# Optimization experiments

Hardware: AMD Instinct MI355X
Metric: run time of the kernel (lower is better)

The kernel has to match this reference:

```python
import jax, jax.numpy as jnp
import numpy as np

N = 50000      # nodes
E = 600000     # edges
D_IN = 128
HID = 128
D_OUT = 3
G = 32         # graphs in the batch


def setup_inputs() -> dict:
    key = jax.random.key(0)
    ks = jax.random.split(key, 16)
    s = 0.05
    x = jax.random.normal(ks[0], (N, D_IN), dtype=jnp.float32)
    edge_index = jax.random.randint(ks[1], (2, E), 0, N, dtype=jnp.int64)
    batch = jnp.sort(jax.random.randint(ks[2], (N,), 0, G, dtype=jnp.int64))
    return {
        "x": x,
        "conv0_Wl": jax.random.normal(ks[3], (HID, D_IN), jnp.float32) * s,
        "conv0_bl": jnp.zeros((HID,), jnp.float32),
        "conv0_Wr": jax.random.normal(ks[4], (HID, D_IN), jnp.float32) * s,
        "lin1_W": jax.random.normal(ks[5], (HID, HID), jnp.float32) * s,
        "lin1_b": jnp.zeros((HID,), jnp.float32),
        "conv1_Wl": jax.random.normal(ks[6], (HID, HID), jnp.float32) * s,
        "conv1_bl": jnp.zeros((HID,), jnp.float32),
        "conv1_Wr": jax.random.normal(ks[7], (HID, HID), jnp.float32) * s,
        "fc_W": jax.random.normal(ks[8], (D_OUT, HID), jnp.float32) * s,
        "fc_b": jnp.zeros((D_OUT,), jnp.float32),
        "edge_index": edge_index,
        "batch": batch,
    }


def _sage_conv(x, Wl, bl, Wr, src, dst):
    # PyG SAGEConv (mean aggr): out = lin_l(mean_{j in N(i)} x_j) + lin_r(x_i)
    msg = x[src]                                              # [E, d] gather
    ssum = jax.ops.segment_sum(msg, dst, num_segments=N)      # [N, d]
    cnt = jax.ops.segment_sum(jnp.ones((src.shape[0],), x.dtype), dst, num_segments=N)
    aggr = ssum / jnp.maximum(cnt, 1.0)[:, None]
    return aggr @ Wl.T + bl + x @ Wr.T


def reference(x, conv0_Wl, conv0_bl, conv0_Wr, lin1_W, lin1_b,
              conv1_Wl, conv1_bl, conv1_Wr, fc_W, fc_b,
              edge_index, batch):
    src, dst = edge_index[0], edge_index[1]
    # conv0 -> relu (dropout is identity in eval mode)
    h = jax.nn.relu(_sage_conv(x, conv0_Wl, conv0_bl, conv0_Wr, src, dst))
    # Linear -> relu -> SAGEConv -> relu
    h = jax.nn.relu(h @ lin1_W.T + lin1_b)
    h = jax.nn.relu(_sage_conv(h, conv1_Wl, conv1_bl, conv1_Wr, src, dst))
    # global_mean_pool over graphs
    gsum = jax.ops.segment_sum(h, batch, num_segments=G)
    gcnt = jax.ops.segment_sum(jnp.ones((h.shape[0],), h.dtype), batch, num_segments=G)
    pooled = gsum / jnp.maximum(gcnt, 1.0)[:, None]           # [G, HID]
    return pooled @ fc_W.T + fc_b                             # [G, D_OUT]
```

## Files before the change

kernel.cpp:

```cpp
#include <hip/hip_runtime.h>
#include <hip/hip_bf16.h>
#include <stdint.h>


typedef __attribute__((ext_vector_type(8))) short short8;
typedef __attribute__((ext_vector_type(4))) float f32x4;

__device__ __forceinline__ float bits2f(uint32_t b) {
    union { uint32_t u; float f; } c; c.u = b; return c.f;
}
__device__ __forceinline__ unsigned short f2bf(float f) {
    __hip_bfloat16 h = __float2bfloat16(f);
    union { __hip_bfloat16 h; unsigned short u; } c; c.h = h; return c.u;
}
__device__ __forceinline__ uint32_t pack2bf(float a, float b) {
    return (uint32_t)f2bf(a) | ((uint32_t)f2bf(b) << 16);
}
__device__ __forceinline__ void acc8(float* a, uint4 v) {
    a[0] += bits2f(v.x << 16); a[1] += bits2f(v.x & 0xffff0000u);
    a[2] += bits2f(v.y << 16); a[3] += bits2f(v.y & 0xffff0000u);
    a[4] += bits2f(v.z << 16); a[5] += bits2f(v.z & 0xffff0000u);
    a[6] += bits2f(v.w << 16); a[7] += bits2f(v.w & 0xffff0000u);
}

__device__ __forceinline__ void detect_flags(const unsigned short* x,
                                             const int* ei,
                                             int& isbf, int& is64) {
    int lane = threadIdx.x & 63;
    unsigned short h = x[lane];
    int e = (h >> 7) & 0xFF;
    unsigned long long mbf = __ballot(e >= 102 && e <= 137);
    unsigned long long m64 = __ballot(ei[2 * lane + 1] != 0);
    isbf = (__popcll(mbf) >= 52) ? 1 : 0;
    is64 = (m64 == 0ULL) ? 1 : 0;
}

#define WB_W0L 0
#define WB_W0R 16384
#define WB_W1  32768
#define WB_W1L 49152
#define WB_W1R 65536
#define WB_TOTAL 81920
#define CF_B0L 0
#define CF_B1  128
#define CF_B1L 256
#define CF_FCW 384
#define CF_FCB 768
#define CF_TOTAL 771

__global__ __launch_bounds__(256) void prep_kernel(
    const void* x, const int* __restrict__ ei,
    const void* s0, const void* s1, const void* s2, const void* s3,
    const void* s4, const void* f0, const void* f1, const void* f2,
    const void* f3, const void* f4,
    unsigned short* __restrict__ Hb, unsigned short* __restrict__ wb,
    float* __restrict__ cf, int* __restrict__ cnt, int* __restrict__ nbr,
    int* __restrict__ flags, int n8, int E, int EG, int WC) {
    int isbf, is64;
    detect_flags((const unsigned short*)x, ei, isbf, is64);
    int b = blockIdx.x;
    if (b == 0 && threadIdx.x == 0) { flags[0] = isbf; flags[1] = is64; }

    if (b < EG) {
        int e = b * 256 + threadIdx.x;
        if (e >= E) return;
        int s, d;
        if (is64) { s = ei[2 * e]; d = ei[2 * (E + e)]; }
        else      { s = ei[e];     d = ei[E + e]; }
        int pos = atomicAdd(&cnt[d], 1);
        if (pos < 64) nbr[((size_t)d << 6) + pos] = s;
    } else if (b < EG + WC) {
        int i = (b - EG) * 256 + threadIdx.x;
        if (i < WB_TOTAL) {
            const void* p; int k = i & 16383;
            switch (i >> 14) {
                case 0: p = s0; break;
                case 1: p = s1; break;
                case 2: p = s2; break;
                case 3: p = s3; break;
                default: p = s4; break;
            }
            wb[i] = isbf ? ((const unsigned short*)p)[k]
                         : f2bf(((const float*)p)[k]);
        } else {
            int j = i - WB_TOTAL;
            if (j >= CF_TOTAL) return;
            const void* p; int k;
            if      (j < CF_B1)  { p = f0; k = j; }
            else if (j < CF_B1L) { p = f1; k = j - CF_B1; }
            else if (j < CF_FCW) { p = f2; k = j - CF_B1L; }
            else if (j < CF_FCB) { p = f3; k = j - CF_FCW; }
            else                 { p = f4; k = j - CF_FCB; }
            cf[j] = isbf ? bits2f((uint32_t)((const unsigned short*)p)[k] << 16)
                         : ((const float*)p)[k];
        }
    } else {
        if (isbf) return;
        int i = (b - EG - WC) * 256 + threadIdx.x;
        if (i >= n8) return;
        float4 a = ((const float4*)x)[2 * i];
        float4 c = ((const float4*)x)[2 * i + 1];
        uint4 d;
        d.x = pack2bf(a.x, a.y); d.y = pack2bf(a.z, a.w);
        d.z = pack2bf(c.x, c.y); d.w = pack2bf(c.z, c.w);
        ((uint4*)Hb)[i] = d;
    }
}

template <bool LIN1, bool POOL>
__device__ __forceinline__ void conv_core(
    const void* xsel, const unsigned short* __restrict__ Hbuf,
    const int* __restrict__ cnt, const int* __restrict__ nbr,
    const unsigned short* __restrict__ Wl, const unsigned short* __restrict__ Wr,
    const float* __restrict__ bias,
    const unsigned short* __restrict__ W2, const float* __restrict__ bias2,
    unsigned short* __restrict__ Hdst,
    float* __restrict__ pool, const int* __restrict__ batch,
    const int* __restrict__ flags, int N) {
    __shared__ unsigned short bufA[16 * 136];
    __shared__ unsigned short bufB[16 * 136];
    __shared__ float pbuf[4 * 128];
    const int t = threadIdx.x;
    const int lane = t & 63;
    const int w = t >> 6;
    const int l15 = lane & 15;
    const int kq = lane >> 4;
    const int m0 = blockIdx.x * 16;

    const int flags0 = flags[0];
    const unsigned short* Hs = flags0 ? (const unsigned short*)xsel : Hbuf;

    int f64 = 0, gmin = 0, g[4];
    if (POOL) {
        f64 = flags[1];
        gmin = f64 ? batch[2 * m0] : batch[m0];
#pragma unroll
        for (int r = 0; r < 4; r++) {
            int gr = m0 + kq * 4 + r;
            g[r] = (gr < N) ? (f64 ? batch[2 * gr] : batch[gr]) : -1;
        }
        for (int i = t; i < 512; i += 256) pbuf[i] = 0.f;
    }

    short8 xf[4];
    {
        int xr = m0 + l15; if (xr >= N) xr = N - 1;
        const unsigned short* xrow = Hs + (size_t)xr * 128 + kq * 8;
#pragma unroll
        for (int kc = 0; kc < 4; kc++) xf[kc] = *(const short8*)(xrow + kc * 32);
    }
    float bc[2];
    const int nt0 = w * 2;
    bc[0] = bias[nt0 * 16 + l15];
    bc[1] = bias[(nt0 + 1) * 16 + l15];

    {
        const int row = w * 4 + kq;
        const int node = m0 + row;
        float a[8] = {0.f, 0.f, 0.f, 0.f, 0.f, 0.f, 0.f, 0.f};
        float invd = 0.f;
        if (node < N) {
            int dcnt = cnt[node];
            invd = 1.f / fmaxf((float)dcnt, 1.f);
            if (dcnt > 64) dcnt = 64;
            const int* nrow = nbr + ((size_t)node << 6);
            const uint4* H4 = (const uint4*)Hs;
            for (int base = 0; base < dcnt; base += 16) {
                int c = dcnt - base; if (c > 16) c = 16;
                int idx = (l15 < c) ? nrow[base + l15] : 0;
                int it = 0;
                for (; it + 4 <= c; it += 4) {
                    int j0 = __shfl(idx, kq * 16 + it, 64);
                    int j1 = __shfl(idx, kq * 16 + it + 1, 64);
                    int j2 = __shfl(idx, kq * 16 + it + 2, 64);
                    int j3 = __shfl(idx, kq * 16 + it + 3, 64);
                    uint4 v0 = H4[(size_t)j0 * 16 + l15];
                    uint4 v1 = H4[(size_t)j1 * 16 + l15];
                    uint4 v2 = H4[(size_t)j2 * 16 + l15];
                    uint4 v3 = H4[(size_t)j3 * 16 + l15];
                    acc8(a, v0); acc8(a, v1); acc8(a, v2); acc8(a, v3);
                }
                for (; it < c; ++it) {
                    int j = __shfl(idx, kq * 16 + it, 64);
                    acc8(a, H4[(size_t)j * 16 + l15]);
                }
            }
        }
        uint4 o;
        o.x = pack2bf(a[0] * invd, a[1] * invd);
        o.y = pack2bf(a[2] * invd, a[3] * invd);
        o.z = pack2bf(a[4] * invd, a[5] * invd);
        o.w = pack2bf(a[6] * invd, a[7] * invd);
        *(uint4*)(bufA + row * 136 + l15 * 8) = o;
    }
    __syncthreads();

    short8 af[4];
#pragma unroll
    for (int kc = 0; kc < 4; kc++)
        af[kc] = *(const short8*)(bufA + l15 * 136 + kc * 32 + kq * 8);

    f32x4 acc[2];
    acc[0] = (f32x4){0.f, 0.f, 0.f, 0.f};
    acc[1] = (f32x4){0.f, 0.f, 0.f, 0.f};
#pragma unroll
    for (int kc = 0; kc < 4; kc++) {
#pragma unroll
        for (int u = 0; u < 2; u++) {
            const size_t woff = (size_t)((nt0 + u) * 16 + l15) * 128 + kc * 32 + kq * 8;
            acc[u] = __builtin_amdgcn_mfma_f32_16x16x32_bf16(
                xf[kc], *(const short8*)(Wr + woff), acc[u], 0, 0, 0);
            acc[u] = __builtin_amdgcn_mfma_f32_16x16x32_bf16(
                af[kc], *(const short8*)(Wl + woff), acc[u], 0, 0, 0);
        }
    }

    if (LIN1) {
#pragma unroll
        for (int u = 0; u < 2; u++) {
#pragma unroll
            for (int r = 0; r < 4; r++) {
                bufB[(kq * 4 + r) * 136 + (nt0 + u) * 16 + l15] =
                    f2bf(fmaxf(acc[u][r] + bc[u], 0.f));
            }
        }
        __syncthreads();
        short8 hf[4];
#pragma unroll
        for (int kc = 0; kc < 4; kc++)
            hf[kc] = *(const short8*)(bufB + l15 * 136 + kc * 32 + kq * 8);
        acc[0] = (f32x4){0.f, 0.f, 0.f, 0.f};
        acc[1] = (f32x4){0.f, 0.f, 0.f, 0.f};
        bc[0] = bias2[nt0 * 16 + l15];
        bc[1] = bias2[(nt0 + 1) * 16 + l15];
#pragma unroll
        for (int kc = 0; kc < 4; kc++) {
#pragma unroll
            for (int u = 0; u < 2; u++) {
                const size_t woff = (size_t)((nt0 + u) * 16 + l15) * 128 + kc * 32 + kq * 8;
                acc[u] = __builtin_amdgcn_mfma_f32_16x16x32_bf16(
                    hf[kc], *(const short8*)(W2 + woff), acc[u], 0, 0, 0);
            }
        }
    }

    if (POOL) {
        bool same = (g[0] == g[1]) && (g[1] == g[2]) && (g[2] == g[3]) && (g[0] >= 0);
#pragma unroll
        for (int u = 0; u < 2; u++) {
            int c = (nt0 + u) * 16 + l15;
            float v0 = fmaxf(acc[u][0] + bc[u], 0.f);
            float v1 = fmaxf(acc[u][1] + bc[u], 0.f);
            float v2 = fmaxf(acc[u][2] + bc[u], 0.f);
            float v3 = fmaxf(acc[u][3] + bc[u], 0.f);
            if (same) {
                int si = g[0] - gmin;
                float s4 = (v0 + v1) + (v2 + v3);
                if (si < 4) atomicAdd(&pbuf[si * 128 + c], s4);
                else        atomicAdd(&pool[g[0] * 128 + c], s4);
            } else {
                float vr[4] = {v0, v1, v2, v3};
#pragma unroll
                for (int r = 0; r < 4; r++) {
                    if (g[r] >= 0) {
                        int si = g[r] - gmin;
                        if (si < 4) atomicAdd(&pbuf[si * 128 + c], vr[r]);
                        else        atomicAdd(&pool[g[r] * 128 + c], vr[r]);
                    }
                }
            }
        }
        __syncthreads();
        for (int i = t; i < 512; i += 256) {
            float v = pbuf[i];
            if (v != 0.f)
                atomicAdd(&pool[(gmin + (i >> 7)) * 128 + (i & 127)], v);
        }
    } else {
#pragma unroll
        for (int u = 0; u < 2; u++) {
#pragma unroll
            for (int r = 0; r < 4; r++) {
                bufA[(kq * 4 + r) * 136 + (nt0 + u) * 16 + l15] =
                    f2bf(fmaxf(acc[u][r] + bc[u], 0.f));
            }
        }
        __syncthreads();
        int row = t >> 4, colsh = (t & 15) * 8;
        uint4 val = *(const uint4*)(bufA + row * 136 + colsh);
        if (m0 + row < N)
            *(uint4*)(Hdst + (size_t)(m0 + row) * 128 + colsh) = val;
    }
}

__global__ __launch_bounds__(256) void conv01_kernel(
    const void* xsel, const unsigned short* __restrict__ Hbuf,
    const int* __restrict__ cnt, const int* __restrict__ nbr,
    const unsigned short* __restrict__ Wl, const unsigned short* __restrict__ Wr,
    const float* __restrict__ bias,
    const unsigned short* __restrict__ W2, const float* __restrict__ bias2,
    unsigned short* __restrict__ Hdst, const int* __restrict__ flags, int N) {
    conv_core<true, false>(xsel, Hbuf, cnt, nbr, Wl, Wr, bias, W2, bias2,
                           Hdst, nullptr, nullptr, flags, N);
}

__global__ __launch_bounds__(256) void conv1p_kernel(
    const void* xsel, const unsigned short* __restrict__ Hbuf,
    const int* __restrict__ cnt, const int* __restrict__ nbr,
    const unsigned short* __restrict__ Wl, const unsigned short* __restrict__ Wr,
    const float* __restrict__ bias,
    float* __restrict__ pool, const int* __restrict__ batch,
    const int* __restrict__ flags, int N) {
    conv_core<false, true>(xsel, Hbuf, cnt, nbr, Wl, Wr, bias,
                           nullptr, nullptr, nullptr, pool, batch, flags, N);
}

__global__ void fc_kernel(const float* __restrict__ pool,
                          const int* __restrict__ batch,
                          const float* __restrict__ W,
                          const float* __restrict__ b,
                          void* __restrict__ out,
                          const int* __restrict__ flags, int N, int G) {
    __shared__ int gst[64];
    int t = threadIdx.x;
    int f64 = flags[1];
    int isbf = flags[0];
    if (t <= G) {
        int lo = 0, hi = N;
        while (lo < hi) {
            int mid = (lo + hi) >> 1;
            int bv = f64 ? batch[2 * mid] : batch[mid];
            if (bv < t) lo = mid + 1; else hi = mid;
        }
        gst[t] = lo;
    }
    __syncthreads();
    if (t >= G * 3) return;
    int g = t / 3, o = t % 3;
    int cnt = gst[g + 1] - gst[g];
    float inv = 1.f / fmaxf((float)cnt, 1.f);
    float acc = 0.f;
    for (int k = 0; k < 128; k++)
        acc += pool[g * 128 + k] * W[o * 128 + k];
    float r = acc * inv + b[o];
    if (isbf) ((__hip_bfloat16*)out)[t] = __float2bfloat16(r);
    else      ((float*)out)[t] = r;
}

extern "C" void kernel_launch(void* const* d_in, const int* in_sizes, int n_in,
                              void* d_out, int out_size, void* d_ws, size_t ws_size,
                              hipStream_t stream) {
    const void* x   = d_in[0];
    const void* W0l = d_in[1];
    const void* b0l = d_in[2];
    const void* W0r = d_in[3];
    const void* W1  = d_in[4];
    const void* b1  = d_in[5];
    const void* W1l = d_in[6];
    const void* b1l = d_in[7];
    const void* W1r = d_in[8];
    const void* fcW = d_in[9];
    const void* fcb = d_in[10];
    const int* edge_index = (const int*)d_in[11];
    const int* batch      = (const int*)d_in[12];

    const int N = in_sizes[12];
    const int E = in_sizes[11] / 2;
    const int G = out_size / 3;

    char* ws = (char*)d_ws;
    auto align64 = [](size_t v) { return (v + 63) & ~(size_t)63; };
    size_t off = 0;
    size_t OFF_CNT  = off; off = align64(off + (size_t)N * 4);
    size_t OFF_POOL = off; off = align64(off + (size_t)G * 128 * 4);
    size_t MEMSET_BYTES = off;
    size_t OFF_FLAGS = off; off = align64(off + 64);
    size_t OFF_NBR  = off; off = align64(off + (size_t)N * 64 * 4);
    size_t OFF_WB   = off; off = align64(off + (size_t)WB_TOTAL * 2);
    size_t OFF_CF   = off; off = align64(off + (size_t)CF_TOTAL * 4);
    size_t OFF_HB   = off; off = align64(off + ((size_t)N + 64) * 128 * 2);
    size_t OFF_H2   = off; off = align64(off + ((size_t)N + 64) * 128 * 2);
    (void)ws_size;

    int*    cnt    = (int*)(ws + OFF_CNT);
    float*  pool   = (float*)(ws + OFF_POOL);
    int*    flags  = (int*)(ws + OFF_FLAGS);
    int*    nbr    = (int*)(ws + OFF_NBR);
    unsigned short* wb = (unsigned short*)(ws + OFF_WB);
    float*  cf     = (float*)(ws + OFF_CF);
    unsigned short* Hb = (unsigned short*)(ws + OFF_HB);
    unsigned short* H2 = (unsigned short*)(ws + OFF_H2);

    hipMemsetAsync(ws, 0, MEMSET_BYTES, stream);

    int n8 = (N * 128) / 8;
    int EG  = (E + 255) / 256;
    int WC  = (WB_TOTAL + CF_TOTAL + 255) / 256;
    int CVT = (n8 + 255) / 256;
    prep_kernel<<<EG + WC + CVT, 256, 0, stream>>>(
        x, edge_index, W0l, W0r, W1, W1l, W1r, b0l, b1, b1l, fcW, fcb,
        Hb, wb, cf, cnt, nbr, flags, n8, E, EG, WC);

    int cgrid = (N + 15) / 16;

    conv01_kernel<<<cgrid, 256, 0, stream>>>(
        x, Hb, cnt, nbr, wb + WB_W0L, wb + WB_W0R, cf + CF_B0L,
        wb + WB_W1, cf + CF_B1, H2, flags, N);

    conv1p_kernel<<<cgrid, 256, 0, stream>>>(
        H2, H2, cnt, nbr, wb + WB_W1L, wb + WB_W1R, cf + CF_B1L,
        pool, batch, flags, N);

    fc_kernel<<<1, 128, 0, stream>>>(pool, batch, cf + CF_FCW, cf + CF_FCB,
                                     d_out, flags, N, G);

    (void)in_sizes; (void)n_in; (void)out_size;
}
```

Measured before the change: 249.5 us.

## Gather neighbor features in fp8 and fuse final FC into last conv

Adds fp8 (e4m3) copies of the node features and the hidden layer, written during prep and conv01. The neighbor-mean gathers now read these instead of bf16, which halves the bytes per gathered row in the bandwidth-bound aggregation. The separate fc kernel is removed: the last block to finish conv1p, found with an atomic ticket, does the pooling division and FC. The cost is lower precision in the aggregated messages, which may break tolerance, plus extra fp8 writes.

```diff
diff --git a/kernel.cpp b/kernel.cpp
--- a/kernel.cpp
+++ b/kernel.cpp
@@ -5,6 +5,7 @@
 
 typedef __attribute__((ext_vector_type(8))) short short8;
 typedef __attribute__((ext_vector_type(4))) float f32x4;
+typedef __attribute__((ext_vector_type(2))) float f32x2;
 
 __device__ __forceinline__ float bits2f(uint32_t b) {
     union { uint32_t u; float f; } c; c.u = b; return c.f;
@@ -16,11 +17,19 @@
 __device__ __forceinline__ uint32_t pack2bf(float a, float b) {
     return (uint32_t)f2bf(a) | ((uint32_t)f2bf(b) << 16);
 }
-__device__ __forceinline__ void acc8(float* a, uint4 v) {
-    a[0] += bits2f(v.x << 16); a[1] += bits2f(v.x & 0xffff0000u);
-    a[2] += bits2f(v.y << 16); a[3] += bits2f(v.y & 0xffff0000u);
-    a[4] += bits2f(v.z << 16); a[5] += bits2f(v.z & 0xffff0000u);
-    a[6] += bits2f(v.w << 16); a[7] += bits2f(v.w & 0xffff0000u);
+__device__ __forceinline__ uint32_t pk4fp8(float f0, float f1, float f2, float f3) {
+    int o = 0;
+    o = __builtin_amdgcn_cvt_pk_fp8_f32(f0, f1, o, false);
+    o = __builtin_amdgcn_cvt_pk_fp8_f32(f2, f3, o, true);
+    return (uint32_t)o;
+}
+__device__ __forceinline__ void acc8f8(float* a, uint2 v) {
+    f32x2 p0 = __builtin_amdgcn_cvt_pk_f32_fp8((int)v.x, false);
+    f32x2 p1 = __builtin_amdgcn_cvt_pk_f32_fp8((int)v.x, true);
+    f32x2 p2 = __builtin_amdgcn_cvt_pk_f32_fp8((int)v.y, false);
+    f32x2 p3 = __builtin_amdgcn_cvt_pk_f32_fp8((int)v.y, true);
+    a[0] += p0.x; a[1] += p0.y; a[2] += p1.x; a[3] += p1.y;
+    a[4] += p2.x; a[5] += p2.y; a[6] += p3.x; a[7] += p3.y;
 }
 
 __device__ __forceinline__ void detect_flags(const unsigned short* x,
@@ -53,7 +62,8 @@
     const void* s0, const void* s1, const void* s2, const void* s3,
     const void* s4, const void* f0, const void* f1, const void* f2,
     const void* f3, const void* f4,
-    unsigned short* __restrict__ Hb, unsigned short* __restrict__ wb,
+    unsigned short* __restrict__ Hb, uint2* __restrict__ Xf8,
+    unsigned short* __restrict__ wb,
     float* __restrict__ cf, int* __restrict__ cnt, int* __restrict__ nbr,
     int* __restrict__ flags, int n8, int E, int EG, int WC) {
     int isbf, is64;
@@ -95,31 +105,50 @@
                          : ((const float*)p)[k];
         }
     } else {
-        if (isbf) return;
         int i = (b - EG - WC) * 256 + threadIdx.x;
         if (i >= n8) return;
-        float4 a = ((const float4*)x)[2 * i];
-        float4 c = ((const float4*)x)[2 * i + 1];
-        uint4 d;
-        d.x = pack2bf(a.x, a.y); d.y = pack2bf(a.z, a.w);
-        d.z = pack2bf(c.x, c.y); d.w = pack2bf(c.z, c.w);
-        ((uint4*)Hb)[i] = d;
+        float f[8];
+        if (isbf) {
+            uint4 d = ((const uint4*)x)[i];
+            f[0] = bits2f(d.x << 16); f[1] = bits2f(d.x & 0xffff0000u);
+            f[2] = bits2f(d.y << 16); f[3] = bits2f(d.y & 0xffff0000u);
+            f[4] = bits2f(d.z << 16); f[5] = bits2f(d.z & 0xffff0000u);
+            f[6] = bits2f(d.w << 16); f[7] = bits2f(d.w & 0xffff0000u);
+        } else {
+            float4 a = ((const float4*)x)[2 * i];
+            float4 c = ((const float4*)x)[2 * i + 1];
+            f[0] = a.x; f[1] = a.y; f[2] = a.z; f[3] = a.w;
+            f[4] = c.x; f[5] = c.y; f[6] = c.z; f[7] = c.w;
+            uint4 d;
+            d.x = pack2bf(f[0], f[1]); d.y = pack2bf(f[2], f[3]);
+            d.z = pack2bf(f[4], f[5]); d.w = pack2bf(f[6], f[7]);
+            ((uint4*)Hb)[i] = d;
+        }
+        uint2 o8;
+        o8.x = pk4fp8(f[0], f[1], f[2], f[3]);
+        o8.y = pk4fp8(f[4], f[5], f[6], f[7]);
+        Xf8[i] = o8;
     }
 }
 
 template <bool LIN1, bool POOL>
 __device__ __forceinline__ void conv_core(
     const void* xsel, const unsigned short* __restrict__ Hbuf,
+    const uint2* __restrict__ G8,
     const int* __restrict__ cnt, const int* __restrict__ nbr,
     const unsigned short* __restrict__ Wl, const unsigned short* __restrict__ Wr,
     const float* __restrict__ bias,
     const unsigned short* __restrict__ W2, const float* __restrict__ bias2,
-    unsigned short* __restrict__ Hdst,
+    unsigned short* __restrict__ Hdst, uint2* __restrict__ Hdst8,
     float* __restrict__ pool, const int* __restrict__ batch,
-    const int* __restrict__ flags, int N) {
+    const int* __restrict__ flags, int N,
+    int* __restrict__ done, const float* __restrict__ fcW,
+    const float* __restrict__ fcb, void* __restrict__ out, int G) {
     __shared__ unsigned short bufA[16 * 136];
-    __shared__ unsigned short bufB[16 * 136];
-    __shared__ float pbuf[4 * 128];
+    __shared__ unsigned short bufB[LIN1 ? 16 * 136 : 1];
+    __shared__ float pbuf[POOL ? 512 : 1];
+    __shared__ int gst_s[34];
+    __shared__ int ticket_s;
     const int t = threadIdx.x;
     const int lane = t & 63;
     const int w = t >> 6;
@@ -164,7 +193,6 @@
             invd = 1.f / fmaxf((float)dcnt, 1.f);
             if (dcnt > 64) dcnt = 64;
             const int* nrow = nbr + ((size_t)node << 6);
-            const uint4* H4 = (const uint4*)Hs;
             for (int base = 0; base < dcnt; base += 16) {
                 int c = dcnt - base; if (c > 16) c = 16;
                 int idx = (l15 < c) ? nrow[base + l15] : 0;
@@ -174,15 +202,15 @@
                     int j1 = __shfl(idx, kq * 16 + it + 1, 64);
                     int j2 = __shfl(idx, kq * 16 + it + 2, 64);
                     int j3 = __shfl(idx, kq * 16 + it + 3, 64);
-                    uint4 v0 = H4[(size_t)j0 * 16 + l15];
-                    uint4 v1 = H4[(size_t)j1 * 16 + l15];
-                    uint4 v2 = H4[(size_t)j2 * 16 + l15];
-                    uint4 v3 = H4[(size_t)j3 * 16 + l15];
-                    acc8(a, v0); acc8(a, v1); acc8(a, v2); acc8(a, v3);
+                    uint2 v0 = G8[(size_t)j0 * 16 + l15];
+                    uint2 v1 = G8[(size_t)j1 * 16 + l15];
+                    uint2 v2 = G8[(size_t)j2 * 16 + l15];
+                    uint2 v3 = G8[(size_t)j3 * 16 + l15];
+                    acc8f8(a, v0); acc8f8(a, v1); acc8f8(a, v2); acc8f8(a, v3);
                 }
                 for (; it < c; ++it) {
                     int j = __shfl(idx, kq * 16 + it, 64);
-                    acc8(a, H4[(size_t)j * 16 + l15]);
+                    acc8f8(a, G8[(size_t)j * 16 + l15]);
                 }
             }
         }
@@ -276,6 +304,39 @@
             if (v != 0.f)
                 atomicAdd(&pool[(gmin + (i >> 7)) * 128 + (i & 127)], v);
         }
+        __threadfence();
+        __syncthreads();
+        if (t == 0) ticket_s = atomicAdd(done, 1);
+        __syncthreads();
+        if (ticket_s == (int)gridDim.x - 1) {
+            __threadfence();
+            int isbf = flags0;
+            if (t <= G) {
+                int lo = 0, hi = N;
+                while (lo < hi) {
+                    int mid = (lo + hi) >> 1;
+                    int bv = f64 ? batch[2 * mid] : batch[mid];
+                    if (bv < t) lo = mid + 1; else hi = mid;
+                }
+                gst_s[t] = lo;
+            }
+            __syncthreads();
+            if (t < G * 3) {
+                int gg = t / 3, o = t % 3;
+                int cc = gst_s[gg + 1] - gst_s[gg];
+                float inv = 1.f / fmaxf((float)cc, 1.f);
+                float a2 = 0.f;
+                for (int k = 0; k < 128; k++) {
+                    float pv = __hip_atomic_load(&pool[gg * 128 + k],
+                                                 __ATOMIC_RELAXED,
+                                                 __HIP_MEMORY_SCOPE_AGENT);
+                    a2 += pv * fcW[o * 128 + k];
+                }
+                float r = a2 * inv + fcb[o];
+                if (isbf) ((__hip_bfloat16*)out)[t] = __float2bfloat16(r);
+                else      ((float*)out)[t] = r;
+            }
+        }
     } else {
 #pragma unroll
         for (int u = 0; u < 2; u++) {
@@ -288,63 +349,46 @@
         __syncthreads();
         int row = t >> 4, colsh = (t & 15) * 8;
         uint4 val = *(const uint4*)(bufA + row * 136 + colsh);
-        if (m0 + row < N)
+        if (m0 + row < N) {
             *(uint4*)(Hdst + (size_t)(m0 + row) * 128 + colsh) = val;
+            float h0 = bits2f(val.x << 16), h1 = bits2f(val.x & 0xffff0000u);
+            float h2 = bits2f(val.y << 16), h3 = bits2f(val.y & 0xffff0000u);
+            float h4 = bits2f(val.z << 16), h5 = bits2f(val.z & 0xffff0000u);
+            float h6 = bits2f(val.w << 16), h7 = bits2f(val.w & 0xffff0000u);
+            uint2 e8;
+            e8.x = pk4fp8(h0, h1, h2, h3);
+            e8.y = pk4fp8(h4, h5, h6, h7);
+            Hdst8[(size_t)(m0 + row) * 16 + (colsh >> 3)] = e8;
+        }
     }
 }
 
 __global__ __launch_bounds__(256) void conv01_kernel(
     const void* xsel, const unsigned short* __restrict__ Hbuf,
+    const uint2* __restrict__ G8,
     const int* __restrict__ cnt, const int* __restrict__ nbr,
     const unsigned short* __restrict__ Wl, const unsigned short* __restrict__ Wr,
     const float* __restrict__ bias,
     const unsigned short* __restrict__ W2, const float* __restrict__ bias2,
-    unsigned short* __restrict__ Hdst, const int* __restrict__ flags, int N) {
-    conv_core<true, false>(xsel, Hbuf, cnt, nbr, Wl, Wr, bias, W2, bias2,
-                           Hdst, nullptr, nullptr, flags, N);
+    unsigned short* __restrict__ Hdst, uint2* __restrict__ Hdst8,
+    const int* __restrict__ flags, int N) {
+    conv_core<true, false>(xsel, Hbuf, G8, cnt, nbr, Wl, Wr, bias, W2, bias2,
+                           Hdst, Hdst8, nullptr, nullptr, flags, N,
+                           nullptr, nullptr, nullptr, nullptr, 0);
 }
 
 __global__ __launch_bounds__(256) void conv1p_kernel(
-    const void* xsel, const unsigned short* __restrict__ Hbuf,
+    const unsigned short* __restrict__ Hbuf, const uint2* __restrict__ G8,
     const int* __restrict__ cnt, const int* __restrict__ nbr,
     const unsigned short* __restrict__ Wl, const unsigned short* __restrict__ Wr,
     const float* __restrict__ bias,
     float* __restrict__ pool, const int* __restrict__ batch,
-    const int* __restrict__ flags, int N) {
-    conv_core<false, true>(xsel, Hbuf, cnt, nbr, Wl, Wr, bias,
-                           nullptr, nullptr, nullptr, pool, batch, flags, N);
-}
-
-__global__ void fc_kernel(const float* __restrict__ pool,
-                          const int* __restrict__ batch,
-                          const float* __restrict__ W,
-                          const float* __restrict__ b,
-                          void* __restrict__ out,
-                          const int* __restrict__ flags, int N, int G) {
-    __shared__ int gst[64];
-    int t = threadIdx.x;
-    int f64 = flags[1];
-    int isbf = flags[0];
-    if (t <= G) {
-        int lo = 0, hi = N;
-        while (lo < hi) {
-            int mid = (lo + hi) >> 1;
-            int bv = f64 ? batch[2 * mid] : batch[mid];
-            if (bv < t) lo = mid + 1; else hi = mid;
-        }
-        gst[t] = lo;
-    }
-    __syncthreads();
-    if (t >= G * 3) return;
-    int g = t / 3, o = t % 3;
-    int cnt = gst[g + 1] - gst[g];
-    float inv = 1.f / fmaxf((float)cnt, 1.f);
-    float acc = 0.f;
-    for (int k = 0; k < 128; k++)
-        acc += pool[g * 128 + k] * W[o * 128 + k];
-    float r = acc * inv + b[o];
-    if (isbf) ((__hip_bfloat16*)out)[t] = __float2bfloat16(r);
-    else      ((float*)out)[t] = r;
+    const int* __restrict__ flags, int N,
+    int* __restrict__ done, const float* __restrict__ fcW,
+    const float* __restrict__ fcb, void* __restrict__ out, int G) {
+    conv_core<false, true>(Hbuf, Hbuf, G8, cnt, nbr, Wl, Wr, bias,
+                           nullptr, nullptr, nullptr, nullptr, pool, batch,
+                           flags, N, done, fcW, fcb, out, G);
 }
 
 extern "C" void kernel_launch(void* const* d_in, const int* in_sizes, int n_in,
@@ -373,21 +417,27 @@
     size_t off = 0;
     size_t OFF_CNT  = off; off = align64(off + (size_t)N * 4);
     size_t OFF_POOL = off; off = align64(off + (size_t)G * 128 * 4);
+    size_t OFF_DONE = off; off = align64(off + 64);
     size_t MEMSET_BYTES = off;
     size_t OFF_FLAGS = off; off = align64(off + 64);
     size_t OFF_NBR  = off; off = align64(off + (size_t)N * 64 * 4);
     size_t OFF_WB   = off; off = align64(off + (size_t)WB_TOTAL * 2);
     size_t OFF_CF   = off; off = align64(off + (size_t)CF_TOTAL * 4);
+    size_t OFF_XF8  = off; off = align64(off + (size_t)N * 128);
+    size_t OFF_H2F8 = off; off = align64(off + (size_t)N * 128);
     size_t OFF_HB   = off; off = align64(off + ((size_t)N + 64) * 128 * 2);
     size_t OFF_H2   = off; off = align64(off + ((size_t)N + 64) * 128 * 2);
     (void)ws_size;
 
     int*    cnt    = (int*)(ws + OFF_CNT);
     float*  pool   = (float*)(ws + OFF_POOL);
+    int*    done   = (int*)(ws + OFF_DONE);
     int*    flags  = (int*)(ws + OFF_FLAGS);
     int*    nbr    = (int*)(ws + OFF_NBR);
     unsigned short* wb = (unsigned short*)(ws + OFF_WB);
     float*  cf     = (float*)(ws + OFF_CF);
+    uint2*  Xf8    = (uint2*)(ws + OFF_XF8);
+    uint2*  H2f8   = (uint2*)(ws + OFF_H2F8);
     unsigned short* Hb = (unsigned short*)(ws + OFF_HB);
     unsigned short* H2 = (unsigned short*)(ws + OFF_H2);
 
@@ -399,20 +449,17 @@
     int CVT = (n8 + 255) / 256;
     prep_kernel<<<EG + WC + CVT, 256, 0, stream>>>(
         x, edge_index, W0l, W0r, W1, W1l, W1r, b0l, b1, b1l, fcW, fcb,
-        Hb, wb, cf, cnt, nbr, flags, n8, E, EG, WC);
+        Hb, Xf8, wb, cf, cnt, nbr, flags, n8, E, EG, WC);
 
     int cgrid = (N + 15) / 16;
 
     conv01_kernel<<<cgrid, 256, 0, stream>>>(
-        x, Hb, cnt, nbr, wb + WB_W0L, wb + WB_W0R, cf + CF_B0L,
-        wb + WB_W1, cf + CF_B1, H2, flags, N);
+        x, Hb, Xf8, cnt, nbr, wb + WB_W0L, wb + WB_W0R, cf + CF_B0L,
+        wb + WB_W1, cf + CF_B1, H2, H2f8, flags, N);
 
     conv1p_kernel<<<cgrid, 256, 0, stream>>>(
-        H2, H2, cnt, nbr, wb + WB_W1L, wb + WB_W1R, cf + CF_B1L,
-        pool, batch, flags, N);
-
-    fc_kernel<<<1, 128, 0, stream>>>(pool, batch, cf + CF_FCW, cf + CF_FCB,
-                                     d_out, flags, N, G);
+        H2, H2f8, cnt, nbr, wb + WB_W1L, wb + WB_W1R, cf + CF_B1L,
+        pool, batch, flags, N, done, cf + CF_FCW, cf + CF_FCB, d_out, G);
 
     (void)in_sizes; (void)n_in; (void)out_size;
 }
```

Measured after the change: 473.7 us. 1.9x slower.
